# Performance work log

Hardware: AMD Instinct MI355X
Metric: run time of the kernel (lower is better)

Reference implementation:

```python
import jax, jax.numpy as jnp
import numpy as np

N = 50000
E = 800000
D_IN = 128
D_H = 128
D_OUT = 1


def setup_inputs() -> dict:
    key = jax.random.key(0)
    ks = jax.random.split(key, 12)
    x = jax.random.normal(ks[0], (N, D_IN), dtype=jnp.float32)
    edge_index = jax.random.randint(ks[1], (2, E), 0, N, dtype=jnp.int64)
    def glorot(k, shape):
        lim = float(np.sqrt(6.0 / (shape[0] + shape[1])))
        return jax.random.uniform(k, shape, jnp.float32, -lim, lim)
    return {
        "x": x,
        "edge_index": edge_index,
        "W1": glorot(ks[2], (D_IN, D_H)),  "b1": jnp.zeros((D_H,), jnp.float32),
        "W2": glorot(ks[3], (D_H, D_H)),   "b2": jnp.zeros((D_H,), jnp.float32),
        "W3": glorot(ks[4], (D_H, D_H)),   "b3": jnp.zeros((D_H,), jnp.float32),
        "Wfc": glorot(ks[5], (D_H, D_OUT)), "bfc": jnp.zeros((D_OUT,), jnp.float32),
    }


def _gcn_norm(edge_index, num_nodes):
    # Add self-loops (PyG GCNConv default) and compute symmetric normalization
    loops = jnp.arange(num_nodes, dtype=edge_index.dtype)
    src = jnp.concatenate([edge_index[0], loops])
    dst = jnp.concatenate([edge_index[1], loops])
    ones = jnp.ones(src.shape[0], dtype=jnp.float32)
    deg = jax.ops.segment_sum(ones, dst, num_segments=num_nodes)
    dinv = jnp.where(deg > 0, jax.lax.rsqrt(deg), 0.0)
    norm = dinv[src] * dinv[dst]  # [E + N]
    return src, dst, norm


def _gcn_layer(x, W, b, src, dst, norm, num_nodes):
    xw = x @ W                              # [N, out] dense transform first
    msg = xw[src] * norm[:, None]           # gather + scale
    agg = jax.ops.segment_sum(msg, dst, num_segments=num_nodes)  # scatter-add
    return agg + b


def reference(x, edge_index, W1, b1, W2, b2, W3, b3, Wfc, bfc):
    num_nodes = x.shape[0]
    src, dst, norm = _gcn_norm(edge_index, num_nodes)
    h = jax.nn.relu(_gcn_layer(x, W1, b1, src, dst, norm, num_nodes))
    h = jax.nn.relu(_gcn_layer(h, W2, b2, src, dst, norm, num_nodes))
    h = jax.nn.relu(_gcn_layer(h, W3, b3, src, dst, norm, num_nodes))
    return h @ Wfc + bfc  # [N, 1]
```

## Files before the change

### kernel.cpp

```cpp
#include <hip/hip_runtime.h>

#define D 128
#define SCAN_ELEMS 4096

typedef __attribute__((ext_vector_type(8))) short short8;
typedef __attribute__((ext_vector_type(4))) float f32x4;

__device__ inline void f2bf(float f, short& hi, short& lo) {
    union { float f; unsigned u; } a; a.f = f;
    unsigned r = a.u + 0x7fffu + ((a.u >> 16) & 1u);
    hi = (short)(r >> 16);
    union { unsigned u; float f; } h; h.u = ((unsigned)(unsigned short)hi) << 16;
    union { float f; unsigned u; } b; b.f = f - h.f;
    unsigned r2 = b.u + 0x7fffu + ((b.u >> 16) & 1u);
    lo = (short)(r2 >> 16);
}

__device__ inline unsigned enc24(float f) {
    union { float f; unsigned u; } a; a.f = f;
    unsigned r = a.u + 0x7fu + ((a.u >> 8) & 1u);
    return r >> 8;
}

__device__ inline void g24(const unsigned short* __restrict__ xh,
                           const unsigned char* __restrict__ xl,
                           int row, int c, float4& a) {
    unsigned off = ((unsigned)row << 7) + (unsigned)c;
    uint2 h2 = *reinterpret_cast<const uint2*>(xh + off);
    unsigned lb = *reinterpret_cast<const unsigned*>(xl + off);
    union { unsigned u; float f; } v0, v1, v2, v3;
    v0.u = __builtin_amdgcn_perm(h2.x, lb, 0x0504000Cu);
    v1.u = __builtin_amdgcn_perm(h2.x, lb, 0x0706010Cu);
    v2.u = __builtin_amdgcn_perm(h2.y, lb, 0x0504020Cu);
    v3.u = __builtin_amdgcn_perm(h2.y, lb, 0x0706030Cu);
    a.x += v0.f; a.y += v1.f; a.z += v2.f; a.w += v3.f;
}


__device__ void wsplit_body(int tid, const float* __restrict__ W1,
                            const float* __restrict__ W2, const float* __restrict__ W3,
                            short* __restrict__ Bsw) {
    int layer = tid >> 14;
    int rem = tid & 16383;
    int k = rem >> 7, c = rem & 127;
    const float* Wg = (layer == 0) ? W1 : ((layer == 1) ? W2 : W3);
    float v = Wg[k * 128 + c];
    short hi, lo; f2bf(v, hi, lo);
    int ktile = k >> 5, kk = k & 31, q = kk >> 3, j = kk & 7;
    int ct = c >> 4, mm = c & 15, lane = q * 16 + mm;
    int idx = layer * 32768 + ((ktile * 8 + ct) * 64 + lane) * 8 + j;
    Bsw[idx] = hi;
    Bsw[idx + 16384] = lo;
}

__global__ __launch_bounds__(256) void count_wsplit_kernel(const int* __restrict__ dst,
                                                           int* __restrict__ deg,
                                                           unsigned short* __restrict__ rank,
                                                           int e, int nbCount,
                                                           const float* __restrict__ W1,
                                                           const float* __restrict__ W2,
                                                           const float* __restrict__ W3,
                                                           short* __restrict__ Bsw) {
    if ((int)blockIdx.x < nbCount) {
        int i = blockIdx.x * 256 + threadIdx.x;
        if (i < e) rank[i] = (unsigned short)atomicAdd(&deg[dst[i]], 1);
    } else {
        int tid = (blockIdx.x - nbCount) * 256 + threadIdx.x;
        wsplit_body(tid, W1, W2, W3, Bsw);
    }
}

__global__ __launch_bounds__(256) void scanA_kernel(const int* __restrict__ deg,
                                                    int* __restrict__ blkSums, int n) {
    __shared__ int waveSums[4];
    int t = threadIdx.x;
    int base = blockIdx.x * SCAN_ELEMS + t * 16;
    int s = 0;
    if (base + 16 <= n) {
        const int4* p = reinterpret_cast<const int4*>(deg + base);
        #pragma unroll
        for (int k = 0; k < 4; ++k) {
            int4 v = p[k];
            s += v.x + v.y + v.z + v.w;
        }
    } else {
        for (int k = 0; k < 16; ++k) {
            int i = base + k;
            if (i < n) s += deg[i];
        }
    }
    #pragma unroll
    for (int off = 32; off > 0; off >>= 1) s += __shfl_down(s, off);
    int lane = t & 63, w = t >> 6;
    if (lane == 0) waveSums[w] = s;
    __syncthreads();
    if (t == 0) blkSums[blockIdx.x] = waveSums[0] + waveSums[1] + waveSums[2] + waveSums[3];
}

__global__ __launch_bounds__(256) void scanC_kernel(const int* __restrict__ deg,
                                                    const int* __restrict__ blkSums,
                                                    int* __restrict__ offsets,
                                                    float* __restrict__ dinv, int n, int nblk) {
    __shared__ int waveSums[4];
    __shared__ int blkBase;
    int t = threadIdx.x;
    int lane = t & 63, w = t >> 6;

    if (t < 64) {
        int s = (t < nblk && t < (int)blockIdx.x) ? blkSums[t] : 0;
        #pragma unroll
        for (int off = 32; off > 0; off >>= 1) s += __shfl_down(s, off);
        if (t == 0) blkBase = s;
    }

    int base = blockIdx.x * SCAN_ELEMS + t * 16;
    int v[16];
    int s = 0;
    #pragma unroll
    for (int k = 0; k < 16; ++k) {
        int i = base + k;
        int d = (i < n) ? deg[i] : 0;
        v[k] = d;
        s += d;
    }
    int incl = s;
    #pragma unroll
    for (int off = 1; off < 64; off <<= 1) {
        int u = __shfl_up(incl, off);
        if (lane >= off) incl += u;
    }
    if (lane == 63) waveSums[w] = incl;
    __syncthreads();
    int waveOff = 0;
    for (int i = 0; i < 4; ++i) if (i < w) waveOff += waveSums[i];
    int off0 = blkBase + waveOff + incl - s;

    #pragma unroll
    for (int k = 0; k < 16; ++k) {
        int i = base + k;
        if (i < n) {
            offsets[i] = off0;
            dinv[i] = rsqrtf((float)(v[k] + 1));
            off0 += v[k];
        }
    }
}

__device__ void gemm_body(int blk, const float* __restrict__ A,
                          const short* __restrict__ Bsw,
                          const float* __restrict__ dinv,
                          unsigned short* __restrict__ xh,
                          unsigned char* __restrict__ xl, int n, int t) {
    int w = t >> 6;
    int lane = t & 63;
    int quad = lane >> 4;
    int m = lane & 15;

    int rowBase = blk * 64 + w * 16;
    int arow = rowBase + m;
    bool valid = arow < n;
    const float* ap = A + (size_t)(valid ? arow : 0) * D + quad * 8;

    f32x4 acc[8];
    #pragma unroll
    for (int ct = 0; ct < 8; ++ct) acc[ct] = (f32x4){0.f, 0.f, 0.f, 0.f};

    #pragma unroll
    for (int kt = 0; kt < 4; ++kt) {
        short8 a_hi, a_lo;
        {
            float4 f0 = *reinterpret_cast<const float4*>(ap + kt * 32);
            float4 f1 = *reinterpret_cast<const float4*>(ap + kt * 32 + 4);
            float fv[8] = {f0.x, f0.y, f0.z, f0.w, f1.x, f1.y, f1.z, f1.w};
            #pragma unroll
            for (int j = 0; j < 8; ++j) {
                short h, l; f2bf(valid ? fv[j] : 0.f, h, l);
                a_hi[j] = h; a_lo[j] = l;
            }
        }
        const short* bp = Bsw + (kt * 512 + lane) * 8;
        #pragma unroll
        for (int ct = 0; ct < 8; ++ct) {
            short8 b_hi = *reinterpret_cast<const short8*>(bp + ct * 512);
            short8 b_lo = *reinterpret_cast<const short8*>(bp + 16384 + ct * 512);
            acc[ct] = __builtin_amdgcn_mfma_f32_16x16x32_bf16(a_hi, b_hi, acc[ct], 0, 0, 0);
            acc[ct] = __builtin_amdgcn_mfma_f32_16x16x32_bf16(a_hi, b_lo, acc[ct], 0, 0, 0);
            acc[ct] = __builtin_amdgcn_mfma_f32_16x16x32_bf16(a_lo, b_hi, acc[ct], 0, 0, 0);
        }
    }

    #pragma unroll
    for (int r = 0; r < 4; ++r) {
        int row = rowBase + quad * 4 + r;
        if (row < n) {
            float s = dinv[row];
            size_t rb = (size_t)row * 128 + m;
            #pragma unroll
            for (int ct = 0; ct < 8; ++ct) {
                unsigned e24 = enc24(acc[ct][r] * s);
                xh[rb + ct * 16] = (unsigned short)(e24 >> 8);
                xl[rb + ct * 16] = (unsigned char)(e24 & 0xffu);
            }
        }
    }
}

__global__ __launch_bounds__(256) void gemm_kernel(const float* __restrict__ A,
                                                   const short* __restrict__ Bsw,
                                                   const float* __restrict__ dinv,
                                                   unsigned short* __restrict__ xh,
                                                   unsigned char* __restrict__ xl, int n) {
    gemm_body(blockIdx.x, A, Bsw, dinv, xh, xl, n, threadIdx.x);
}

__global__ __launch_bounds__(256) void fill_gemm_kernel(const int* __restrict__ src,
                                                        const int* __restrict__ dst,
                                                        const int* __restrict__ offsets,
                                                        const unsigned short* __restrict__ rank,
                                                        unsigned short* __restrict__ csr_src,
                                                        int e, int nbFill,
                                                        const float* __restrict__ A,
                                                        const short* __restrict__ Bsw,
                                                        const float* __restrict__ dinv,
                                                        unsigned short* __restrict__ xh,
                                                        unsigned char* __restrict__ xl, int n) {
    if ((int)blockIdx.x < nbFill) {
        int i = blockIdx.x * 256 + threadIdx.x;
        if (i < e) csr_src[offsets[dst[i]] + rank[i]] = (unsigned short)src[i];
    } else {
        gemm_body(blockIdx.x - nbFill, A, Bsw, dinv, xh, xl, n, threadIdx.x);
    }
}

__global__ __launch_bounds__(256) void agg_kernel(const unsigned short* __restrict__ xh,
                                                  const unsigned char* __restrict__ xl,
                                                  const unsigned short* __restrict__ csr_src,
                                                  const int* __restrict__ offsets,
                                                  const int* __restrict__ deg,
                                                  const float* __restrict__ dinv,
                                                  const float* __restrict__ bias,
                                                  float* __restrict__ outp,
                                                  const float* __restrict__ fcw,
                                                  const float* __restrict__ fcb,
                                                  float* __restrict__ fcout,
                                                  int n) {
    int wave = (blockIdx.x * blockDim.x + threadIdx.x) >> 6;
    int lane = threadIdx.x & 63;
    if (wave >= n) return;
    int node = wave;
    int half = lane >> 5;
    int l32  = lane & 31;
    int col  = l32 << 2;

    int base = offsets[node];
    int cnt  = deg[node];

    float di = dinv[node];
    float4 vs = make_float4(0.f, 0.f, 0.f, 0.f);
    g24(xh, xl, node, col, vs);
    float4 b = *reinterpret_cast<const float4*>(bias + col);

    float4 acc0 = make_float4(0.f, 0.f, 0.f, 0.f);
    float4 acc1 = make_float4(0.f, 0.f, 0.f, 0.f);
    float4 acc2 = make_float4(0.f, 0.f, 0.f, 0.f);
    float4 acc3 = make_float4(0.f, 0.f, 0.f, 0.f);

    if (cnt <= 64) {
        int idx = (lane < cnt) ? (int)csr_src[base + lane] : 0;
        int j = 0;
        for (; j + 8 <= cnt; j += 8) {
            int s0 = __shfl(idx, j     + half);
            int s1 = __shfl(idx, j + 2 + half);
            int s2 = __shfl(idx, j + 4 + half);
            int s3 = __shfl(idx, j + 6 + half);
            g24(xh, xl, s0, col, acc0);
            g24(xh, xl, s1, col, acc1);
            g24(xh, xl, s2, col, acc2);
            g24(xh, xl, s3, col, acc3);
        }
        for (; j + 2 <= cnt; j += 2) {
            int s0 = __shfl(idx, j + half);
            g24(xh, xl, s0, col, acc0);
        }
        if (j < cnt) {
            int s0 = __shfl(idx, j);
            if (half == 0) g24(xh, xl, s0, col, acc1);
        }
    } else {
        int j = 0;
        for (; j + 2 <= cnt; j += 2) {
            int s = (int)csr_src[base + j + half];
            g24(xh, xl, s, col, acc0);
        }
        if (j < cnt && half == 0) {
            int s = (int)csr_src[base + j];
            g24(xh, xl, s, col, acc1);
        }
    }

    acc0.x += acc1.x + acc2.x + acc3.x;
    acc0.y += acc1.y + acc2.y + acc3.y;
    acc0.z += acc1.z + acc2.z + acc3.z;
    acc0.w += acc1.w + acc2.w + acc3.w;
    acc0.x += __shfl_down(acc0.x, 32);
    acc0.y += __shfl_down(acc0.y, 32);
    acc0.z += __shfl_down(acc0.z, 32);
    acc0.w += __shfl_down(acc0.w, 32);

    float4 r;
    r.x = fmaxf(di * (acc0.x + vs.x) + b.x, 0.f);
    r.y = fmaxf(di * (acc0.y + vs.y) + b.y, 0.f);
    r.z = fmaxf(di * (acc0.z + vs.z) + b.z, 0.f);
    r.w = fmaxf(di * (acc0.w + vs.w) + b.w, 0.f);

    if (fcw == nullptr) {
        if (half == 0)
            *reinterpret_cast<float4*>(outp + (size_t)node * D + col) = r;
    } else {
        float4 wv = *reinterpret_cast<const float4*>(fcw + col);
        float s = (half == 0) ? (r.x * wv.x + r.y * wv.y + r.z * wv.z + r.w * wv.w) : 0.f;
        #pragma unroll
        for (int off = 32; off > 0; off >>= 1) s += __shfl_down(s, off);
        if (lane == 0) fcout[node] = s + fcb[0];
    }
}


extern "C" void kernel_launch(void* const* d_in, const int* in_sizes, int n_in,
                              void* d_out, int out_size, void* d_ws, size_t ws_size,
                              hipStream_t stream) {
    const float* x   = (const float*)d_in[0];
    const int*   ei  = (const int*)d_in[1];
    const float* W1  = (const float*)d_in[2];
    const float* b1  = (const float*)d_in[3];
    const float* W2  = (const float*)d_in[4];
    const float* b2  = (const float*)d_in[5];
    const float* W3  = (const float*)d_in[6];
    const float* b3  = (const float*)d_in[7];
    const float* Wfc = (const float*)d_in[8];
    const float* bfc = (const float*)d_in[9];
    float* outp = (float*)d_out;

    const int n = in_sizes[0] / D;
    const int e = in_sizes[1] / 2;
    const int* src = ei;
    const int* dst = ei + e;

    char* ws = (char*)d_ws;
    size_t off = 0;
    auto alloc = [&](size_t bytes) {
        void* p = ws + off;
        off += (bytes + 255) & ~(size_t)255;
        return p;
    };
    int*            deg     = (int*)alloc((size_t)n * 4);
    size_t          zero_bytes = off;
    int*            offsets = (int*)alloc((size_t)n * 4);
    float*          dinv    = (float*)alloc((size_t)n * 4);
    int*            blkSums = (int*)alloc(64 * 4);
    short*          Bsw     = (short*)alloc((size_t)3 * 32768 * 2);
    unsigned short* rank    = (unsigned short*)alloc((size_t)e * 2);
    unsigned short* csr_src = (unsigned short*)alloc((size_t)e * 2);
    unsigned short* xhbuf   = (unsigned short*)alloc((size_t)n * 128 * 2);
    unsigned char*  xlbuf   = (unsigned char*)alloc((size_t)n * 128);
    float*          buf1    = (float*)alloc((size_t)n * D * 4);

    int eb256 = (e + 255) / 256;
    int scan_blocks = (n + SCAN_ELEMS - 1) / SCAN_ELEMS;
    int gemm_blocks = (n + 63) / 64;
    int agg_blocks  = (n + 3) / 4;

    hipMemsetAsync(ws, 0, zero_bytes, stream);
    count_wsplit_kernel<<<eb256 + 192, 256, 0, stream>>>(dst, deg, rank, e, eb256,
                                                         W1, W2, W3, Bsw);
    scanA_kernel<<<scan_blocks, 256, 0, stream>>>(deg, blkSums, n);
    scanC_kernel<<<scan_blocks, 256, 0, stream>>>(deg, blkSums, offsets, dinv, n, scan_blocks);
    fill_gemm_kernel<<<eb256 + gemm_blocks, 256, 0, stream>>>(src, dst, offsets, rank, csr_src,
                                                              e, eb256, x, Bsw, dinv,
                                                              xhbuf, xlbuf, n);
    agg_kernel<<<agg_blocks, 256, 0, stream>>>(xhbuf, xlbuf, csr_src, offsets, deg, dinv, b1, buf1,
                                               nullptr, nullptr, nullptr, n);
    gemm_kernel<<<gemm_blocks, 256, 0, stream>>>(buf1, Bsw + 32768, dinv, xhbuf, xlbuf, n);
    agg_kernel<<<agg_blocks, 256, 0, stream>>>(xhbuf, xlbuf, csr_src, offsets, deg, dinv, b2, buf1,
                                               nullptr, nullptr, nullptr, n);
    gemm_kernel<<<gemm_blocks, 256, 0, stream>>>(buf1, Bsw + 65536, dinv, xhbuf, xlbuf, n);
    agg_kernel<<<agg_blocks, 256, 0, stream>>>(xhbuf, xlbuf, csr_src, offsets, deg, dinv, b3, nullptr,
                                               Wfc, bfc, outp, n);
}
```

Measured before the change: 329.9 us.

## Column-chunk the packed 24-bit features and aggregate per chunk for cache locality

Splits the 24-bit feature buffer into 8 column chunks of 16 features, each stored as 64-byte rows with the high and low bytes packed together. The aggregation kernel is rewritten so each block handles one chunk for 32 nodes, with 16 edge slots per wave, so the gathered working set per chunk (about 3.2 MB) fits in cache. The final FC output is pre-filled with the bias in the scan kernel and accumulated with atomics across chunks. The cost is eight passes over the CSR indices and one atomic per node per chunk in the last layer.

Result: slower. 589.9 us (+78.8%).

```diff
diff --git a/kernel.cpp b/kernel.cpp
--- a/kernel.cpp
+++ b/kernel.cpp
@@ -22,12 +22,10 @@
     return r >> 8;
 }
 
-__device__ inline void g24(const unsigned short* __restrict__ xh,
-                           const unsigned char* __restrict__ xl,
-                           int row, int c, float4& a) {
-    unsigned off = ((unsigned)row << 7) + (unsigned)c;
-    uint2 h2 = *reinterpret_cast<const uint2*>(xh + off);
-    unsigned lb = *reinterpret_cast<const unsigned*>(xl + off);
+__device__ inline void g24p(const unsigned char* __restrict__ cb, int row, int cg, float4& a) {
+    const unsigned char* p = cb + ((size_t)row << 6);
+    uint2 h2 = *reinterpret_cast<const uint2*>(p + cg * 8);
+    unsigned lb = *reinterpret_cast<const unsigned*>(p + 32 + cg * 4);
     union { unsigned u; float f; } v0, v1, v2, v3;
     v0.u = __builtin_amdgcn_perm(h2.x, lb, 0x0504000Cu);
     v1.u = __builtin_amdgcn_perm(h2.x, lb, 0x0706010Cu);
@@ -100,7 +98,9 @@
 __global__ __launch_bounds__(256) void scanC_kernel(const int* __restrict__ deg,
                                                     const int* __restrict__ blkSums,
                                                     int* __restrict__ offsets,
-                                                    float* __restrict__ dinv, int n, int nblk) {
+                                                    float* __restrict__ dinv, int n, int nblk,
+                                                    float* __restrict__ fcout,
+                                                    const float* __restrict__ fcb) {
     __shared__ int waveSums[4];
     __shared__ int blkBase;
     int t = threadIdx.x;
@@ -135,12 +135,14 @@
     for (int i = 0; i < 4; ++i) if (i < w) waveOff += waveSums[i];
     int off0 = blkBase + waveOff + incl - s;
 
+    float b0 = fcb[0];
     #pragma unroll
     for (int k = 0; k < 16; ++k) {
         int i = base + k;
         if (i < n) {
             offsets[i] = off0;
             dinv[i] = rsqrtf((float)(v[k] + 1));
+            fcout[i] = b0;
             off0 += v[k];
         }
     }
@@ -149,8 +151,7 @@
 __device__ void gemm_body(int blk, const float* __restrict__ A,
                           const short* __restrict__ Bsw,
                           const float* __restrict__ dinv,
-                          unsigned short* __restrict__ xh,
-                          unsigned char* __restrict__ xl, int n, int t) {
+                          unsigned char* __restrict__ xp, int n, int t) {
     int w = t >> 6;
     int lane = t & 63;
     int quad = lane >> 4;
@@ -194,12 +195,12 @@
         int row = rowBase + quad * 4 + r;
         if (row < n) {
             float s = dinv[row];
-            size_t rb = (size_t)row * 128 + m;
             #pragma unroll
             for (int ct = 0; ct < 8; ++ct) {
                 unsigned e24 = enc24(acc[ct][r] * s);
-                xh[rb + ct * 16] = (unsigned short)(e24 >> 8);
-                xl[rb + ct * 16] = (unsigned char)(e24 & 0xffu);
+                unsigned char* p = xp + (((size_t)ct * n + row) << 6);
+                *reinterpret_cast<unsigned short*>(p + 2 * m) = (unsigned short)(e24 >> 8);
+                p[32 + m] = (unsigned char)(e24 & 0xffu);
             }
         }
     }
@@ -208,9 +209,8 @@
 __global__ __launch_bounds__(256) void gemm_kernel(const float* __restrict__ A,
                                                    const short* __restrict__ Bsw,
                                                    const float* __restrict__ dinv,
-                                                   unsigned short* __restrict__ xh,
-                                                   unsigned char* __restrict__ xl, int n) {
-    gemm_body(blockIdx.x, A, Bsw, dinv, xh, xl, n, threadIdx.x);
+                                                   unsigned char* __restrict__ xp, int n) {
+    gemm_body(blockIdx.x, A, Bsw, dinv, xp, n, threadIdx.x);
 }
 
 __global__ __launch_bounds__(256) void fill_gemm_kernel(const int* __restrict__ src,
@@ -222,106 +222,75 @@
                                                         const float* __restrict__ A,
                                                         const short* __restrict__ Bsw,
                                                         const float* __restrict__ dinv,
-                                                        unsigned short* __restrict__ xh,
-                                                        unsigned char* __restrict__ xl, int n) {
+                                                        unsigned char* __restrict__ xp, int n) {
     if ((int)blockIdx.x < nbFill) {
         int i = blockIdx.x * 256 + threadIdx.x;
         if (i < e) csr_src[offsets[dst[i]] + rank[i]] = (unsigned short)src[i];
     } else {
-        gemm_body(blockIdx.x - nbFill, A, Bsw, dinv, xh, xl, n, threadIdx.x);
-    }
-}
-
-__global__ __launch_bounds__(256) void agg_kernel(const unsigned short* __restrict__ xh,
-                                                  const unsigned char* __restrict__ xl,
-                                                  const unsigned short* __restrict__ csr_src,
-                                                  const int* __restrict__ offsets,
-                                                  const int* __restrict__ deg,
-                                                  const float* __restrict__ dinv,
-                                                  const float* __restrict__ bias,
-                                                  float* __restrict__ outp,
-                                                  const float* __restrict__ fcw,
-                                                  const float* __restrict__ fcb,
-                                                  float* __restrict__ fcout,
-                                                  int n) {
-    int wave = (blockIdx.x * blockDim.x + threadIdx.x) >> 6;
-    int lane = threadIdx.x & 63;
-    if (wave >= n) return;
-    int node = wave;
-    int half = lane >> 5;
-    int l32  = lane & 31;
-    int col  = l32 << 2;
-
-    int base = offsets[node];
-    int cnt  = deg[node];
-
-    float di = dinv[node];
-    float4 vs = make_float4(0.f, 0.f, 0.f, 0.f);
-    g24(xh, xl, node, col, vs);
-    float4 b = *reinterpret_cast<const float4*>(bias + col);
-
-    float4 acc0 = make_float4(0.f, 0.f, 0.f, 0.f);
-    float4 acc1 = make_float4(0.f, 0.f, 0.f, 0.f);
-    float4 acc2 = make_float4(0.f, 0.f, 0.f, 0.f);
-    float4 acc3 = make_float4(0.f, 0.f, 0.f, 0.f);
-
-    if (cnt <= 64) {
-        int idx = (lane < cnt) ? (int)csr_src[base + lane] : 0;
-        int j = 0;
-        for (; j + 8 <= cnt; j += 8) {
-            int s0 = __shfl(idx, j     + half);
-            int s1 = __shfl(idx, j + 2 + half);
-            int s2 = __shfl(idx, j + 4 + half);
-            int s3 = __shfl(idx, j + 6 + half);
-            g24(xh, xl, s0, col, acc0);
-            g24(xh, xl, s1, col, acc1);
-            g24(xh, xl, s2, col, acc2);
-            g24(xh, xl, s3, col, acc3);
-        }
-        for (; j + 2 <= cnt; j += 2) {
-            int s0 = __shfl(idx, j + half);
-            g24(xh, xl, s0, col, acc0);
-        }
-        if (j < cnt) {
-            int s0 = __shfl(idx, j);
-            if (half == 0) g24(xh, xl, s0, col, acc1);
-        }
-    } else {
-        int j = 0;
-        for (; j + 2 <= cnt; j += 2) {
-            int s = (int)csr_src[base + j + half];
-            g24(xh, xl, s, col, acc0);
-        }
-        if (j < cnt && half == 0) {
-            int s = (int)csr_src[base + j];
-            g24(xh, xl, s, col, acc1);
-        }
-    }
-
-    acc0.x += acc1.x + acc2.x + acc3.x;
-    acc0.y += acc1.y + acc2.y + acc3.y;
-    acc0.z += acc1.z + acc2.z + acc3.z;
-    acc0.w += acc1.w + acc2.w + acc3.w;
-    acc0.x += __shfl_down(acc0.x, 32);
-    acc0.y += __shfl_down(acc0.y, 32);
-    acc0.z += __shfl_down(acc0.z, 32);
-    acc0.w += __shfl_down(acc0.w, 32);
-
-    float4 r;
-    r.x = fmaxf(di * (acc0.x + vs.x) + b.x, 0.f);
-    r.y = fmaxf(di * (acc0.y + vs.y) + b.y, 0.f);
-    r.z = fmaxf(di * (acc0.z + vs.z) + b.z, 0.f);
-    r.w = fmaxf(di * (acc0.w + vs.w) + b.w, 0.f);
-
-    if (fcw == nullptr) {
-        if (half == 0)
-            *reinterpret_cast<float4*>(outp + (size_t)node * D + col) = r;
-    } else {
-        float4 wv = *reinterpret_cast<const float4*>(fcw + col);
-        float s = (half == 0) ? (r.x * wv.x + r.y * wv.y + r.z * wv.z + r.w * wv.w) : 0.f;
+        gemm_body(blockIdx.x - nbFill, A, Bsw, dinv, xp, n, threadIdx.x);
+    }
+}
+
+template<bool FC>
+__global__ __launch_bounds__(256) void aggc_kernel(const unsigned char* __restrict__ xp,
+                                                   const unsigned short* __restrict__ csr,
+                                                   const int* __restrict__ offsets,
+                                                   const int* __restrict__ deg,
+                                                   const float* __restrict__ dinv,
+                                                   const float* __restrict__ bias,
+                                                   float* __restrict__ outp,
+                                                   const float* __restrict__ fcw,
+                                                   float* __restrict__ fcout,
+                                                   int n) {
+    int chunk = blockIdx.x & 7;
+    int grp = blockIdx.x >> 3;
+    int t = threadIdx.x;
+    int wv = t >> 6, lane = t & 63;
+    int eslot = lane >> 2, cg = lane & 3;
+
+    const unsigned char* cb = xp + ((size_t)chunk * n << 6);
+    float4 bv = *reinterpret_cast<const float4*>(bias + chunk * 16 + cg * 4);
+    float4 wvv;
+    if (FC) wvv = *reinterpret_cast<const float4*>(fcw + chunk * 16 + cg * 4);
+
+    int node0 = grp * 32 + wv * 8;
+    for (int i = 0; i < 8; ++i) {
+        int node = node0 + i;
+        if (node >= n) break;
+        int base = offsets[node];
+        int cnt  = deg[node];
+
+        float4 acc = make_float4(0.f, 0.f, 0.f, 0.f);
+        for (int j = 0; j < cnt; j += 16) {
+            int ee = j + eslot;
+            if (ee < cnt) g24p(cb, (int)csr[base + ee], cg, acc);
+        }
+        if (eslot == 0) g24p(cb, node, cg, acc);
+
         #pragma unroll
-        for (int off = 32; off > 0; off >>= 1) s += __shfl_down(s, off);
-        if (lane == 0) fcout[node] = s + fcb[0];
+        for (int off = 4; off < 64; off <<= 1) {
+            acc.x += __shfl_xor(acc.x, off);
+            acc.y += __shfl_xor(acc.y, off);
+            acc.z += __shfl_xor(acc.z, off);
+            acc.w += __shfl_xor(acc.w, off);
+        }
+
+        float di = dinv[node];
+        float4 r;
+        r.x = fmaxf(di * acc.x + bv.x, 0.f);
+        r.y = fmaxf(di * acc.y + bv.y, 0.f);
+        r.z = fmaxf(di * acc.z + bv.z, 0.f);
+        r.w = fmaxf(di * acc.w + bv.w, 0.f);
+
+        if (FC) {
+            float p = r.x * wvv.x + r.y * wvv.y + r.z * wvv.z + r.w * wvv.w;
+            p += __shfl_xor(p, 1);
+            p += __shfl_xor(p, 2);
+            if (lane == 0) atomicAdd(fcout + node, p);
+        } else {
+            if (eslot == 0)
+                *reinterpret_cast<float4*>(outp + (size_t)node * D + chunk * 16 + cg * 4) = r;
+        }
     }
 }
 
@@ -361,29 +330,29 @@
     short*          Bsw     = (short*)alloc((size_t)3 * 32768 * 2);
     unsigned short* rank    = (unsigned short*)alloc((size_t)e * 2);
     unsigned short* csr_src = (unsigned short*)alloc((size_t)e * 2);
-    unsigned short* xhbuf   = (unsigned short*)alloc((size_t)n * 128 * 2);
-    unsigned char*  xlbuf   = (unsigned char*)alloc((size_t)n * 128);
+    unsigned char*  xpack   = (unsigned char*)alloc((size_t)8 * n * 64);
     float*          buf1    = (float*)alloc((size_t)n * D * 4);
 
     int eb256 = (e + 255) / 256;
     int scan_blocks = (n + SCAN_ELEMS - 1) / SCAN_ELEMS;
     int gemm_blocks = (n + 63) / 64;
-    int agg_blocks  = (n + 3) / 4;
+    int agg_grid = ((n + 31) / 32) * 8;
 
     hipMemsetAsync(ws, 0, zero_bytes, stream);
     count_wsplit_kernel<<<eb256 + 192, 256, 0, stream>>>(dst, deg, rank, e, eb256,
                                                          W1, W2, W3, Bsw);
     scanA_kernel<<<scan_blocks, 256, 0, stream>>>(deg, blkSums, n);
-    scanC_kernel<<<scan_blocks, 256, 0, stream>>>(deg, blkSums, offsets, dinv, n, scan_blocks);
+    scanC_kernel<<<scan_blocks, 256, 0, stream>>>(deg, blkSums, offsets, dinv, n, scan_blocks,
+                                                  outp, bfc);
     fill_gemm_kernel<<<eb256 + gemm_blocks, 256, 0, stream>>>(src, dst, offsets, rank, csr_src,
                                                               e, eb256, x, Bsw, dinv,
-                                                              xhbuf, xlbuf, n);
-    agg_kernel<<<agg_blocks, 256, 0, stream>>>(xhbuf, xlbuf, csr_src, offsets, deg, dinv, b1, buf1,
-                                               nullptr, nullptr, nullptr, n);
-    gemm_kernel<<<gemm_blocks, 256, 0, stream>>>(buf1, Bsw + 32768, dinv, xhbuf, xlbuf, n);
-    agg_kernel<<<agg_blocks, 256, 0, stream>>>(xhbuf, xlbuf, csr_src, offsets, deg, dinv, b2, buf1,
-                                               nullptr, nullptr, nullptr, n);
-    gemm_kernel<<<gemm_blocks, 256, 0, stream>>>(buf1, Bsw + 65536, dinv, xhbuf, xlbuf, n);
-    agg_kernel<<<agg_blocks, 256, 0, stream>>>(xhbuf, xlbuf, csr_src, offsets, deg, dinv, b3, nullptr,
-                                               Wfc, bfc, outp, n);
-}
+                                                              xpack, n);
+    aggc_kernel<false><<<agg_grid, 256, 0, stream>>>(xpack, csr_src, offsets, deg, dinv, b1,
+                                                     buf1, nullptr, nullptr, n);
+    gemm_kernel<<<gemm_blocks, 256, 0, stream>>>(buf1, Bsw + 32768, dinv, xpack, n);
+    aggc_kernel<false><<<agg_grid, 256, 0, stream>>>(xpack, csr_src, offsets, deg, dinv, b2,
+                                                     buf1, nullptr, nullptr, n);
+    gemm_kernel<<<gemm_blocks, 256, 0, stream>>>(buf1, Bsw + 65536, dinv, xpack, n);
+    aggc_kernel<true><<<agg_grid, 256, 0, stream>>>(xpack, csr_src, offsets, deg, dinv, b3,
+                                                    nullptr, Wfc, outp, n);
+}
```

## Emit pre-split bf16 hi/lo activations from aggregation and gather 8 columns per lane

Applied to the files above, without the earlier changes.

The aggregation kernel now writes its ReLU output as bf16 hi/lo pairs instead of fp32, so the following GEMM loads MFMA operands directly and skips the per-element split conversion. The aggregation is also restructured: each lane gathers 8 columns (16-byte hi loads), four quarter-waves handle different neighbours in parallel, the self-loop is folded into the neighbour list, and the quarters are combined with xor-shuffles. This changes the intermediate storage from 4 to 4 bytes per element (two shorts) while moving conversion work into the aggregation epilogue. It also aims to raise memory-level parallelism in the gather.

Measured after the change: 322.5 us. 1.02x faster.

```diff
diff --git a/kernel.cpp b/kernel.cpp
--- a/kernel.cpp
+++ b/kernel.cpp
@@ -20,20 +20,6 @@
     union { float f; unsigned u; } a; a.f = f;
     unsigned r = a.u + 0x7fu + ((a.u >> 8) & 1u);
     return r >> 8;
-}
-
-__device__ inline void g24(const unsigned short* __restrict__ xh,
-                           const unsigned char* __restrict__ xl,
-                           int row, int c, float4& a) {
-    unsigned off = ((unsigned)row << 7) + (unsigned)c;
-    uint2 h2 = *reinterpret_cast<const uint2*>(xh + off);
-    unsigned lb = *reinterpret_cast<const unsigned*>(xl + off);
-    union { unsigned u; float f; } v0, v1, v2, v3;
-    v0.u = __builtin_amdgcn_perm(h2.x, lb, 0x0504000Cu);
-    v1.u = __builtin_amdgcn_perm(h2.x, lb, 0x0706010Cu);
-    v2.u = __builtin_amdgcn_perm(h2.y, lb, 0x0504020Cu);
-    v3.u = __builtin_amdgcn_perm(h2.y, lb, 0x0706030Cu);
-    a.x += v0.f; a.y += v1.f; a.z += v2.f; a.w += v3.f;
 }
 
 
@@ -146,7 +132,10 @@
     }
 }
 
+template<bool SPLIT>
 __device__ void gemm_body(int blk, const float* __restrict__ A,
+                          const unsigned short* __restrict__ Ah,
+                          const unsigned short* __restrict__ Al,
                           const short* __restrict__ Bsw,
                           const float* __restrict__ dinv,
                           unsigned short* __restrict__ xh,
@@ -159,7 +148,7 @@
     int rowBase = blk * 64 + w * 16;
     int arow = rowBase + m;
     bool valid = arow < n;
-    const float* ap = A + (size_t)(valid ? arow : 0) * D + quad * 8;
+    int srow = valid ? arow : 0;
 
     f32x4 acc[8];
     #pragma unroll
@@ -168,7 +157,12 @@
     #pragma unroll
     for (int kt = 0; kt < 4; ++kt) {
         short8 a_hi, a_lo;
-        {
+        if (SPLIT) {
+            size_t off = (size_t)srow * D + kt * 32 + quad * 8;
+            a_hi = *reinterpret_cast<const short8*>(Ah + off);
+            a_lo = *reinterpret_cast<const short8*>(Al + off);
+        } else {
+            const float* ap = A + (size_t)srow * D + quad * 8;
             float4 f0 = *reinterpret_cast<const float4*>(ap + kt * 32);
             float4 f1 = *reinterpret_cast<const float4*>(ap + kt * 32 + 4);
             float fv[8] = {f0.x, f0.y, f0.z, f0.w, f1.x, f1.y, f1.z, f1.w};
@@ -205,12 +199,13 @@
     }
 }
 
-__global__ __launch_bounds__(256) void gemm_kernel(const float* __restrict__ A,
-                                                   const short* __restrict__ Bsw,
-                                                   const float* __restrict__ dinv,
-                                                   unsigned short* __restrict__ xh,
-                                                   unsigned char* __restrict__ xl, int n) {
-    gemm_body(blockIdx.x, A, Bsw, dinv, xh, xl, n, threadIdx.x);
+__global__ __launch_bounds__(256) void gemm_split_kernel(const unsigned short* __restrict__ Ah,
+                                                         const unsigned short* __restrict__ Al,
+                                                         const short* __restrict__ Bsw,
+                                                         const float* __restrict__ dinv,
+                                                         unsigned short* __restrict__ xh,
+                                                         unsigned char* __restrict__ xl, int n) {
+    gemm_body<true>(blockIdx.x, nullptr, Ah, Al, Bsw, dinv, xh, xl, n, threadIdx.x);
 }
 
 __global__ __launch_bounds__(256) void fill_gemm_kernel(const int* __restrict__ src,
@@ -228,100 +223,121 @@
         int i = blockIdx.x * 256 + threadIdx.x;
         if (i < e) csr_src[offsets[dst[i]] + rank[i]] = (unsigned short)src[i];
     } else {
-        gemm_body(blockIdx.x - nbFill, A, Bsw, dinv, xh, xl, n, threadIdx.x);
-    }
-}
-
-__global__ __launch_bounds__(256) void agg_kernel(const unsigned short* __restrict__ xh,
-                                                  const unsigned char* __restrict__ xl,
-                                                  const unsigned short* __restrict__ csr_src,
-                                                  const int* __restrict__ offsets,
-                                                  const int* __restrict__ deg,
-                                                  const float* __restrict__ dinv,
-                                                  const float* __restrict__ bias,
-                                                  float* __restrict__ outp,
-                                                  const float* __restrict__ fcw,
-                                                  const float* __restrict__ fcb,
-                                                  float* __restrict__ fcout,
-                                                  int n) {
+        gemm_body<false>(blockIdx.x - nbFill, A, nullptr, nullptr, Bsw, dinv, xh, xl, n, threadIdx.x);
+    }
+}
+
+template<bool FC>
+__global__ __launch_bounds__(256) void aggq_kernel(const unsigned short* __restrict__ xh,
+                                                   const unsigned char* __restrict__ xl,
+                                                   const unsigned short* __restrict__ csr,
+                                                   const int* __restrict__ offsets,
+                                                   const int* __restrict__ deg,
+                                                   const float* __restrict__ dinv,
+                                                   const float* __restrict__ bias,
+                                                   unsigned short* __restrict__ hh,
+                                                   unsigned short* __restrict__ hl,
+                                                   const float* __restrict__ fcw,
+                                                   const float* __restrict__ fcb,
+                                                   float* __restrict__ fcout,
+                                                   int n) {
     int wave = (blockIdx.x * blockDim.x + threadIdx.x) >> 6;
+    if (wave >= n) return;
     int lane = threadIdx.x & 63;
-    if (wave >= n) return;
+    int q = lane >> 4;
+    int s = lane & 15;
     int node = wave;
-    int half = lane >> 5;
-    int l32  = lane & 31;
-    int col  = l32 << 2;
 
     int base = offsets[node];
     int cnt  = deg[node];
 
+    float4 aA0 = make_float4(0.f, 0.f, 0.f, 0.f), aA1 = make_float4(0.f, 0.f, 0.f, 0.f);
+    float4 aB0 = make_float4(0.f, 0.f, 0.f, 0.f), aB1 = make_float4(0.f, 0.f, 0.f, 0.f);
+
+    auto gq = [&](int row, float4& x0, float4& x1) {
+        const unsigned short* hp = xh + ((size_t)row << 7) + s * 8;
+        const unsigned char*  lp = xl + ((size_t)row << 7) + s * 8;
+        uint4 h4 = *reinterpret_cast<const uint4*>(hp);
+        uint2 l2 = *reinterpret_cast<const uint2*>(lp);
+        union { unsigned u; float f; } e0, e1, e2, e3, e4, e5, e6, e7;
+        e0.u = __builtin_amdgcn_perm(h4.x, l2.x, 0x0504000Cu);
+        e1.u = __builtin_amdgcn_perm(h4.x, l2.x, 0x0706010Cu);
+        e2.u = __builtin_amdgcn_perm(h4.y, l2.x, 0x0504020Cu);
+        e3.u = __builtin_amdgcn_perm(h4.y, l2.x, 0x0706030Cu);
+        e4.u = __builtin_amdgcn_perm(h4.z, l2.y, 0x0504000Cu);
+        e5.u = __builtin_amdgcn_perm(h4.z, l2.y, 0x0706010Cu);
+        e6.u = __builtin_amdgcn_perm(h4.w, l2.y, 0x0504020Cu);
+        e7.u = __builtin_amdgcn_perm(h4.w, l2.y, 0x0706030Cu);
+        x0.x += e0.f; x0.y += e1.f; x0.z += e2.f; x0.w += e3.f;
+        x1.x += e4.f; x1.y += e5.f; x1.z += e6.f; x1.w += e7.f;
+    };
+
+    int total = cnt + 1;
+    if (total <= 64) {
+        int idx = (lane < cnt) ? (int)csr[base + lane] : node;
+        for (int j = 0; j < total; j += 8) {
+            int p0 = j + q, p1 = j + 4 + q;
+            int s0 = __shfl(idx, p0 & 63);
+            int s1 = __shfl(idx, p1 & 63);
+            if (p0 < total) gq(s0, aA0, aA1);
+            if (p1 < total) gq(s1, aB0, aB1);
+        }
+    } else {
+        for (int j = 0; j < cnt; j += 8) {
+            int p0 = j + q, p1 = j + 4 + q;
+            if (p0 < cnt) gq((int)csr[base + p0], aA0, aA1);
+            if (p1 < cnt) gq((int)csr[base + p1], aB0, aB1);
+        }
+        if (q == 0) gq(node, aA0, aA1);
+    }
+
+    aA0.x += aB0.x; aA0.y += aB0.y; aA0.z += aB0.z; aA0.w += aB0.w;
+    aA1.x += aB1.x; aA1.y += aB1.y; aA1.z += aB1.z; aA1.w += aB1.w;
+    #pragma unroll
+    for (int off = 16; off < 64; off <<= 1) {
+        aA0.x += __shfl_xor(aA0.x, off);
+        aA0.y += __shfl_xor(aA0.y, off);
+        aA0.z += __shfl_xor(aA0.z, off);
+        aA0.w += __shfl_xor(aA0.w, off);
+        aA1.x += __shfl_xor(aA1.x, off);
+        aA1.y += __shfl_xor(aA1.y, off);
+        aA1.z += __shfl_xor(aA1.z, off);
+        aA1.w += __shfl_xor(aA1.w, off);
+    }
+
     float di = dinv[node];
-    float4 vs = make_float4(0.f, 0.f, 0.f, 0.f);
-    g24(xh, xl, node, col, vs);
-    float4 b = *reinterpret_cast<const float4*>(bias + col);
-
-    float4 acc0 = make_float4(0.f, 0.f, 0.f, 0.f);
-    float4 acc1 = make_float4(0.f, 0.f, 0.f, 0.f);
-    float4 acc2 = make_float4(0.f, 0.f, 0.f, 0.f);
-    float4 acc3 = make_float4(0.f, 0.f, 0.f, 0.f);
-
-    if (cnt <= 64) {
-        int idx = (lane < cnt) ? (int)csr_src[base + lane] : 0;
-        int j = 0;
-        for (; j + 8 <= cnt; j += 8) {
-            int s0 = __shfl(idx, j     + half);
-            int s1 = __shfl(idx, j + 2 + half);
-            int s2 = __shfl(idx, j + 4 + half);
-            int s3 = __shfl(idx, j + 6 + half);
-            g24(xh, xl, s0, col, acc0);
-            g24(xh, xl, s1, col, acc1);
-            g24(xh, xl, s2, col, acc2);
-            g24(xh, xl, s3, col, acc3);
-        }
-        for (; j + 2 <= cnt; j += 2) {
-            int s0 = __shfl(idx, j + half);
-            g24(xh, xl, s0, col, acc0);
-        }
-        if (j < cnt) {
-            int s0 = __shfl(idx, j);
-            if (half == 0) g24(xh, xl, s0, col, acc1);
-        }
-    } else {
-        int j = 0;
-        for (; j + 2 <= cnt; j += 2) {
-            int s = (int)csr_src[base + j + half];
-            g24(xh, xl, s, col, acc0);
-        }
-        if (j < cnt && half == 0) {
-            int s = (int)csr_src[base + j];
-            g24(xh, xl, s, col, acc1);
-        }
-    }
-
-    acc0.x += acc1.x + acc2.x + acc3.x;
-    acc0.y += acc1.y + acc2.y + acc3.y;
-    acc0.z += acc1.z + acc2.z + acc3.z;
-    acc0.w += acc1.w + acc2.w + acc3.w;
-    acc0.x += __shfl_down(acc0.x, 32);
-    acc0.y += __shfl_down(acc0.y, 32);
-    acc0.z += __shfl_down(acc0.z, 32);
-    acc0.w += __shfl_down(acc0.w, 32);
-
-    float4 r;
-    r.x = fmaxf(di * (acc0.x + vs.x) + b.x, 0.f);
-    r.y = fmaxf(di * (acc0.y + vs.y) + b.y, 0.f);
-    r.z = fmaxf(di * (acc0.z + vs.z) + b.z, 0.f);
-    r.w = fmaxf(di * (acc0.w + vs.w) + b.w, 0.f);
-
-    if (fcw == nullptr) {
-        if (half == 0)
-            *reinterpret_cast<float4*>(outp + (size_t)node * D + col) = r;
-    } else {
-        float4 wv = *reinterpret_cast<const float4*>(fcw + col);
-        float s = (half == 0) ? (r.x * wv.x + r.y * wv.y + r.z * wv.z + r.w * wv.w) : 0.f;
+    float4 b0 = *reinterpret_cast<const float4*>(bias + s * 8);
+    float4 b1 = *reinterpret_cast<const float4*>(bias + s * 8 + 4);
+    float r0 = fmaxf(di * aA0.x + b0.x, 0.f);
+    float r1 = fmaxf(di * aA0.y + b0.y, 0.f);
+    float r2 = fmaxf(di * aA0.z + b0.z, 0.f);
+    float r3 = fmaxf(di * aA0.w + b0.w, 0.f);
+    float r4 = fmaxf(di * aA1.x + b1.x, 0.f);
+    float r5 = fmaxf(di * aA1.y + b1.y, 0.f);
+    float r6 = fmaxf(di * aA1.z + b1.z, 0.f);
+    float r7 = fmaxf(di * aA1.w + b1.w, 0.f);
+
+    if (FC) {
+        float4 w0 = *reinterpret_cast<const float4*>(fcw + s * 8);
+        float4 w1 = *reinterpret_cast<const float4*>(fcw + s * 8 + 4);
+        float p = r0 * w0.x + r1 * w0.y + r2 * w0.z + r3 * w0.w
+                + r4 * w1.x + r5 * w1.y + r6 * w1.z + r7 * w1.w;
+        p += __shfl_xor(p, 1);
+        p += __shfl_xor(p, 2);
+        p += __shfl_xor(p, 4);
+        p += __shfl_xor(p, 8);
+        if (lane == 0) fcout[node] = p + fcb[0];
+    } else if (q == 0) {
+        short8 sh, sl;
+        float rv[8] = {r0, r1, r2, r3, r4, r5, r6, r7};
         #pragma unroll
-        for (int off = 32; off > 0; off >>= 1) s += __shfl_down(s, off);
-        if (lane == 0) fcout[node] = s + fcb[0];
+        for (int i = 0; i < 8; ++i) {
+            short h, l; f2bf(rv[i], h, l);
+            sh[i] = h; sl[i] = l;
+        }
+        size_t off = (size_t)node * D + s * 8;
+        *reinterpret_cast<short8*>(hh + off) = sh;
+        *reinterpret_cast<short8*>(hl + off) = sl;
     }
 }
 
@@ -363,7 +379,8 @@
     unsigned short* csr_src = (unsigned short*)alloc((size_t)e * 2);
     unsigned short* xhbuf   = (unsigned short*)alloc((size_t)n * 128 * 2);
     unsigned char*  xlbuf   = (unsigned char*)alloc((size_t)n * 128);
-    float*          buf1    = (float*)alloc((size_t)n * D * 4);
+    unsigned short* hhbuf   = (unsigned short*)alloc((size_t)n * 128 * 2);
+    unsigned short* hlbuf   = (unsigned short*)alloc((size_t)n * 128 * 2);
 
     int eb256 = (e + 255) / 256;
     int scan_blocks = (n + SCAN_ELEMS - 1) / SCAN_ELEMS;
@@ -378,12 +395,14 @@
     fill_gemm_kernel<<<eb256 + gemm_blocks, 256, 0, stream>>>(src, dst, offsets, rank, csr_src,
                                                               e, eb256, x, Bsw, dinv,
                                                               xhbuf, xlbuf, n);
-    agg_kernel<<<agg_blocks, 256, 0, stream>>>(xhbuf, xlbuf, csr_src, offsets, deg, dinv, b1, buf1,
-                                               nullptr, nullptr, nullptr, n);
-    gemm_kernel<<<gemm_blocks, 256, 0, stream>>>(buf1, Bsw + 32768, dinv, xhbuf, xlbuf, n);
-    agg_kernel<<<agg_blocks, 256, 0, stream>>>(xhbuf, xlbuf, csr_src, offsets, deg, dinv, b2, buf1,
-                                               nullptr, nullptr, nullptr, n);
-    gemm_kernel<<<gemm_blocks, 256, 0, stream>>>(buf1, Bsw + 65536, dinv, xhbuf, xlbuf, n);
-    agg_kernel<<<agg_blocks, 256, 0, stream>>>(xhbuf, xlbuf, csr_src, offsets, deg, dinv, b3, nullptr,
-                                               Wfc, bfc, outp, n);
-}
+    aggq_kernel<false><<<agg_blocks, 256, 0, stream>>>(xhbuf, xlbuf, csr_src, offsets, deg, dinv,
+                                                       b1, hhbuf, hlbuf, nullptr, nullptr, nullptr, n);
+    gemm_split_kernel<<<gemm_blocks, 256, 0, stream>>>(hhbuf, hlbuf, Bsw + 32768, dinv,
+                                                       xhbuf, xlbuf, n);
+    aggq_kernel<false><<<agg_blocks, 256, 0, stream>>>(xhbuf, xlbuf, csr_src, offsets, deg, dinv,
+                                                       b2, hhbuf, hlbuf, nullptr, nullptr, nullptr, n);
+    gemm_split_kernel<<<gemm_blocks, 256, 0, stream>>>(hhbuf, hlbuf, Bsw + 65536, dinv,
+                                                       xhbuf, xlbuf, n);
+    aggq_kernel<true><<<agg_blocks, 256, 0, stream>>>(xhbuf, xlbuf, csr_src, offsets, deg, dinv,
+                                                      b3, nullptr, nullptr, Wfc, bfc, outp, n);
+}
```
